# Performance work log

Measured on AMD Instinct MI355X. Metric: run time of the kernel, lower is better.

The kernel has to match this reference:

```python
import jax, jax.numpy as jnp
import numpy as np

NUM_NODES = 25
EMBED_DIM = 64
OUT_SIZE = 2
N_TOTAL = 204800   # 8192 graphs * 25 nodes
N_EDGES = 3276800  # avg degree 16


def setup_inputs() -> dict:
    key = jax.random.key(0)
    ks = jax.random.split(key, 8)
    x = jax.random.normal(ks[0], (N_TOTAL, EMBED_DIM), dtype=jnp.float32)
    # random edges; real graphs are graph-local but math is identical
    edge_index = jax.random.randint(ks[1], (2, N_EDGES), 0, N_TOTAL, dtype=jnp.int32)
    batch = jnp.repeat(jnp.arange(N_TOTAL // NUM_NODES, dtype=jnp.int32), NUM_NODES)
    hid = NUM_NODES * EMBED_DIM  # 1600
    W_conv = jax.random.normal(ks[2], (EMBED_DIM, EMBED_DIM), dtype=jnp.float32) / np.sqrt(EMBED_DIM)
    b_conv = jnp.zeros((EMBED_DIM,), dtype=jnp.float32)
    W1 = jax.random.normal(ks[3], (hid, hid), dtype=jnp.float32) / np.sqrt(hid)
    b1 = jnp.zeros((hid,), dtype=jnp.float32)
    W2 = jax.random.normal(ks[4], (hid, OUT_SIZE), dtype=jnp.float32) / np.sqrt(hid)
    b2 = jnp.zeros((OUT_SIZE,), dtype=jnp.float32)
    return {"x": x, "edge_index": edge_index, "batch": batch,
            "W_conv": W_conv, "b_conv": b_conv,
            "W1": W1, "b1": b1, "W2": W2, "b2": b2}


def reference(x, edge_index, batch, W_conv, b_conv, W1, b1, W2, b2):
    N = x.shape[0]
    # --- GCNConv: add self-loops, symmetric degree norm, transform, scatter-add ---
    loop = jnp.arange(N, dtype=edge_index.dtype)
    src = jnp.concatenate([edge_index[0], loop])
    dst = jnp.concatenate([edge_index[1], loop])
    deg = jax.ops.segment_sum(jnp.ones_like(dst, dtype=x.dtype), dst, num_segments=N)
    dinv = jax.lax.rsqrt(deg)  # deg >= 1 due to self-loops
    norm = dinv[src] * dinv[dst]                       # [E+N]
    h = x @ W_conv                                     # [N, D]
    msg = h[src] * norm[:, None]                       # gather + scale
    h = jax.ops.segment_sum(msg, dst, num_segments=N) + b_conv
    h = jax.nn.relu(h)
    # --- dense head ---
    nb = -(-batch.shape[0] // NUM_NODES)               # ceil
    h = h.reshape(nb, NUM_NODES * EMBED_DIM)           # [B, 1600]
    h = jax.nn.relu(h @ W1 + b1)
    logits = h @ W2 + b2
    return jax.nn.softmax(logits, axis=-1)
```

## Files before the change

kernel.cpp:

```cpp
#include <hip/hip_runtime.h>
#include <hip/hip_bf16.h>
#include <stdint.h>

#define NT   204800
#define NE   3276800
#define ED   64
#define NBG  8192
#define HID  1600
#define HPAD 1664
#define CAP  56
#define NBKT 400
#define BCAP 9216

typedef float  f32x4  __attribute__((ext_vector_type(4)));
typedef __bf16 bf16x8 __attribute__((ext_vector_type(8)));

__device__ __forceinline__ void async_ld16(const void* g, void* l) {
    __builtin_amdgcn_global_load_lds(
        (__attribute__((address_space(1))) const void*)g,
        (__attribute__((address_space(3))) void*)l, 16, 0, 0);
}

__device__ __forceinline__ unsigned short f2bf_raw(float f) {
    __hip_bfloat16 h = __float2bfloat16(f);
    return *(unsigned short*)&h;
}

__global__ void k_initg(int* __restrict__ gcur) {
    int t = threadIdx.x;
    if (t < NBKT) gcur[t] = t * BCAP;
}

__global__ __launch_bounds__(256) void k_part(const int* __restrict__ srcv,
                                              const int* __restrict__ dstv,
                                              int* __restrict__ gcur,
                                              unsigned* __restrict__ rec) {
    __shared__ int hist[NBKT];
    __shared__ int slot[NBKT];
    __shared__ int gofs[NBKT];
    const int t = threadIdx.x;
    const int base = blockIdx.x * (NE / 512);
    for (int i = t; i < NBKT; i += 256) { hist[i] = 0; slot[i] = 0; }
    __syncthreads();
    for (int j = 0; j < 25; ++j) {
        int d = dstv[base + j * 256 + t];
        atomicAdd(&hist[d >> 9], 1);
    }
    __syncthreads();
    for (int i = t; i < NBKT; i += 256) gofs[i] = atomicAdd(&gcur[i], hist[i]);
    __syncthreads();
    for (int j = 0; j < 25; ++j) {
        int i = base + j * 256 + t;
        int d = dstv[i];
        int s = srcv[i];
        int b = d >> 9;
        int ls = atomicAdd(&slot[b], 1);
        int idx = gofs[b] + ls;
        if (idx < (b + 1) * BCAP)
            rec[idx] = ((unsigned)s << 9) | (unsigned)(d & 511);
    }
}

__global__ __launch_bounds__(512) void k_fillb(const int* __restrict__ gcur,
                                               const unsigned* __restrict__ rec,
                                               int* __restrict__ cur,
                                               int* __restrict__ csr,
                                               float* __restrict__ dinv) {
    __shared__ int cnt[512];
    const int t = threadIdx.x;
    const int b = blockIdx.x;
    const int n0 = b * 512;
    cnt[t] = 0;
    __syncthreads();
    const int bstart = b * BCAP;
    int bcnt = gcur[b] - bstart;
    bcnt = (bcnt > BCAP) ? BCAP : bcnt;
    for (int idx = t; idx < bcnt; idx += 512) {
        unsigned r = rec[bstart + idx];
        unsigned rel = r & 511u;
        int ls = atomicAdd(&cnt[rel], 1);
        if (ls < CAP) csr[(size_t)(n0 + rel) * CAP + ls] = (int)(r >> 9);
    }
    __syncthreads();
    int cn = cnt[t];
    cur[n0 + t] = cn;
    dinv[n0 + t] = rsqrtf((float)cn + 1.f);
}

__global__ __launch_bounds__(256) void k_gemm_conv(const float* __restrict__ x,
                                                   const float* __restrict__ Wc,
                                                   const float* __restrict__ dinv,
                                                   __hip_bfloat16* __restrict__ hbs) {
    __shared__ unsigned short Xs[64 * 72];
    __shared__ unsigned short Wt[64 * 72];
    const int t = threadIdx.x;
    const int row0 = blockIdx.x * 64;
#pragma unroll
    for (int i = 0; i < 4; ++i) {
        int idx = i * 256 + t;
        int r = idx >> 4, c4 = (idx & 15) << 2;
        f32x4 wv = ((const f32x4*)Wc)[idx];
        Wt[(c4 + 0) * 72 + r] = f2bf_raw(wv.x);
        Wt[(c4 + 1) * 72 + r] = f2bf_raw(wv.y);
        Wt[(c4 + 2) * 72 + r] = f2bf_raw(wv.z);
        Wt[(c4 + 3) * 72 + r] = f2bf_raw(wv.w);
        f32x4 xv = ((const f32x4*)(x + (size_t)row0 * 64))[idx];
        ushort4 p;
        p.x = f2bf_raw(xv.x);
        p.y = f2bf_raw(xv.y);
        p.z = f2bf_raw(xv.z);
        p.w = f2bf_raw(xv.w);
        *(ushort4*)&Xs[r * 72 + c4] = p;
    }
    __syncthreads();
    const int w = t >> 6, lane = t & 63;
    const int fr = lane & 15, fq = lane >> 4;
    f32x4 acc[4] = {};
#pragma unroll
    for (int kb = 0; kb < 2; ++kb) {
        bf16x8 av = *(const bf16x8*)&Xs[(w * 16 + fr) * 72 + kb * 32 + fq * 8];
#pragma unroll
        for (int j = 0; j < 4; ++j) {
            bf16x8 bv = *(const bf16x8*)&Wt[(j * 16 + fr) * 72 + kb * 32 + fq * 8];
            acc[j] = __builtin_amdgcn_mfma_f32_16x16x32_bf16(av, bv, acc[j], 0, 0, 0);
        }
    }
#pragma unroll
    for (int r = 0; r < 4; ++r) {
        int row = row0 + w * 16 + fq * 4 + r;
        float di = dinv[row];
        unsigned short* dst = (unsigned short*)&hbs[(size_t)row * 64];
#pragma unroll
        for (int j = 0; j < 4; ++j)
            dst[j * 16 + fr] = f2bf_raw(acc[j][r] * di);
    }
}

__global__ __launch_bounds__(256) void k_gather(const int* __restrict__ cur,
                                                const int* __restrict__ csr,
                                                const float* __restrict__ dinv,
                                                const __hip_bfloat16* __restrict__ hbs,
                                                const float* __restrict__ bc,
                                                __hip_bfloat16* __restrict__ Hb) {
    const int lane = threadIdx.x & 63;
    const int d = blockIdx.x * 4 + (threadIdx.x >> 6);
    const float di = dinv[d];
    int cn = cur[d];
    cn = (cn > CAP) ? CAP : cn;
    int me = (lane < cn) ? __builtin_nontemporal_load(&csr[(size_t)d * CAP + lane]) : 0;
    float acc = __bfloat162float(hbs[(size_t)d * ED + lane]);
    int e = 0;
    for (; e + 8 <= cn; e += 8) {
        int s0 = __shfl(me, e,     64);
        int s1 = __shfl(me, e + 1, 64);
        int s2 = __shfl(me, e + 2, 64);
        int s3 = __shfl(me, e + 3, 64);
        int s4 = __shfl(me, e + 4, 64);
        int s5 = __shfl(me, e + 5, 64);
        int s6 = __shfl(me, e + 6, 64);
        int s7 = __shfl(me, e + 7, 64);
        float h0 = __bfloat162float(hbs[(size_t)s0 * ED + lane]);
        float h1 = __bfloat162float(hbs[(size_t)s1 * ED + lane]);
        float h2 = __bfloat162float(hbs[(size_t)s2 * ED + lane]);
        float h3 = __bfloat162float(hbs[(size_t)s3 * ED + lane]);
        float h4 = __bfloat162float(hbs[(size_t)s4 * ED + lane]);
        float h5 = __bfloat162float(hbs[(size_t)s5 * ED + lane]);
        float h6 = __bfloat162float(hbs[(size_t)s6 * ED + lane]);
        float h7 = __bfloat162float(hbs[(size_t)s7 * ED + lane]);
        acc += ((h0 + h1) + (h2 + h3)) + ((h4 + h5) + (h6 + h7));
    }
    for (; e < cn; ++e) {
        int s = __shfl(me, e, 64);
        acc += __bfloat162float(hbs[(size_t)s * ED + lane]);
    }
    Hb[(size_t)d * ED + lane] = __float2bfloat16(fmaxf(bc[lane] + di * acc, 0.f));
}

__global__ void k_convW1(const float* __restrict__ W1, __hip_bfloat16* __restrict__ Bt) {
    __shared__ float tile[64][65];
    const int t = threadIdx.x;
    const int k0 = blockIdx.x * 64;
    const int n0 = blockIdx.y * 64;
#pragma unroll
    for (int i = 0; i < 16; ++i) {
        int lin = i * 256 + t;
        int r = lin >> 6, c = lin & 63;
        int n = n0 + c;
        tile[r][c] = (n < HID) ? W1[(size_t)(k0 + r) * HID + n] : 0.f;
    }
    __syncthreads();
#pragma unroll
    for (int i = 0; i < 16; ++i) {
        int lin = i * 256 + t;
        int nn = lin >> 6, kk = lin & 63;
        Bt[(size_t)(n0 + nn) * HID + k0 + kk] = __float2bfloat16(tile[kk][nn]);
    }
}

__global__ __launch_bounds__(256) void k_gemm1(const __hip_bfloat16* __restrict__ A,
                                               const __hip_bfloat16* __restrict__ Bt,
                                               const float* __restrict__ b1,
                                               __hip_bfloat16* __restrict__ h2) {
    __shared__ unsigned short As[128 * 32];
    __shared__ unsigned short Bs[128 * 32];
    const int t = threadIdx.x;
    const int lane = t & 63;
    const int wave = t >> 6;
    const int bm0 = blockIdx.x * 128;
    const int bn0 = blockIdx.y * 128;
    const int wm = (wave >> 1) * 64;
    const int wn = (wave & 1) * 64;
    const int fr = lane & 15;
    const int fq = lane >> 4;
    const int sr = t >> 2;
    const int sc = (t & 3) * 8;
    const __hip_bfloat16* ga0 = A + (size_t)(bm0 + sr) * HID + sc;
    const __hip_bfloat16* ga1 = A + (size_t)(bm0 + 64 + sr) * HID + sc;
    const __hip_bfloat16* gb0 = Bt + (size_t)(bn0 + sr) * HID + sc;
    const __hip_bfloat16* gb1 = Bt + (size_t)(bn0 + 64 + sr) * HID + sc;
    unsigned short* lA0 = &As[t * 8];
    unsigned short* lA1 = &As[(256 + t) * 8];
    unsigned short* lB0 = &Bs[t * 8];
    unsigned short* lB1 = &Bs[(256 + t) * 8];
    const unsigned short* fa0 = &As[(wm + fr) * 32 + fq * 8];
    const unsigned short* fb0 = &Bs[(wn + fr) * 32 + fq * 8];
    f32x4 acc[4][4] = {};
    for (int k0 = 0; k0 < HID; k0 += 32) {
        async_ld16(ga0, lA0); async_ld16(ga1, lA1);
        async_ld16(gb0, lB0); async_ld16(gb1, lB1);
        ga0 += 32; ga1 += 32; gb0 += 32; gb1 += 32;
        __syncthreads();
        bf16x8 av[4], bv[4];
#pragma unroll
        for (int i = 0; i < 4; ++i) av[i] = *(const bf16x8*)(fa0 + i * 16 * 32);
#pragma unroll
        for (int j = 0; j < 4; ++j) bv[j] = *(const bf16x8*)(fb0 + j * 16 * 32);
#pragma unroll
        for (int i = 0; i < 4; ++i)
#pragma unroll
            for (int j = 0; j < 4; ++j)
                acc[i][j] = __builtin_amdgcn_mfma_f32_16x16x32_bf16(av[i], bv[j], acc[i][j], 0, 0, 0);
        __syncthreads();
    }
#pragma unroll
    for (int j = 0; j < 4; ++j) {
        int n = bn0 + wn + j * 16 + fr;
        if (n < HID) {
            float bias = b1[n];
#pragma unroll
            for (int i = 0; i < 4; ++i) {
#pragma unroll
                for (int r = 0; r < 4; ++r) {
                    int m = bm0 + wm + i * 16 + fq * 4 + r;
                    float v = acc[i][j][r] + bias;
                    h2[(size_t)m * HID + n] = __float2bfloat16(fmaxf(v, 0.f));
                }
            }
        }
    }
}

__global__ void k_head(const __hip_bfloat16* __restrict__ h2, const float* __restrict__ W2,
                       const float* __restrict__ b2, float* __restrict__ out) {
    int g = blockIdx.x * 4 + (threadIdx.x >> 6);
    int lane = threadIdx.x & 63;
    const __hip_bfloat16* row = h2 + (size_t)g * HID;
    float a0 = 0.f, a1 = 0.f;
#pragma unroll
    for (int i = 0; i < 25; ++i) {
        int k = i * 64 + lane;
        float hv = __bfloat162float(row[k]);
        float2 w = ((const float2*)W2)[k];
        a0 += hv * w.x;
        a1 += hv * w.y;
    }
#pragma unroll
    for (int off = 32; off > 0; off >>= 1) {
        a0 += __shfl_down(a0, off, 64);
        a1 += __shfl_down(a1, off, 64);
    }
    if (lane == 0) {
        float l0 = a0 + b2[0], l1 = a1 + b2[1];
        float mx = fmaxf(l0, l1);
        float e0 = expf(l0 - mx), e1 = expf(l1 - mx);
        float s = e0 + e1;
        out[2 * g]     = e0 / s;
        out[2 * g + 1] = e1 / s;
    }
}

extern "C" void kernel_launch(void* const* d_in, const int* in_sizes, int n_in,
                              void* d_out, int out_size, void* d_ws, size_t ws_size,
                              hipStream_t stream) {
    const float* x  = (const float*)d_in[0];
    const int*   ei = (const int*)d_in[1];
    const float* Wc = (const float*)d_in[3];
    const float* bc = (const float*)d_in[4];
    const float* W1 = (const float*)d_in[5];
    const float* b1 = (const float*)d_in[6];
    const float* W2 = (const float*)d_in[7];
    const float* b2 = (const float*)d_in[8];
    float* out = (float*)d_out;

    const int* srcv = ei;
    const int* dstv = ei + NE;

    char* ws = (char*)d_ws;
    int*   cur  = (int*)ws;
    float* dinv = (float*)(ws + 819200);
    int*   gcur = (int*)(ws + 1638400);
    int*   csr  = (int*)(ws + 1642496);
    unsigned* rec = (unsigned*)(ws + 47517696);
    __hip_bfloat16* hbs = (__hip_bfloat16*)(ws + 47517696);
    __hip_bfloat16* h2  = (__hip_bfloat16*)(ws + 47517696);
    __hip_bfloat16* Hb  = (__hip_bfloat16*)(ws + 73732096);
    __hip_bfloat16* Bt  = (__hip_bfloat16*)(ws + 99946496);

    k_initg    <<<1, 512, 0, stream>>>(gcur);
    k_part     <<<512, 256, 0, stream>>>(srcv, dstv, gcur, rec);
    k_fillb    <<<NBKT, 512, 0, stream>>>(gcur, rec, cur, csr, dinv);
    k_gemm_conv<<<NT / 64, 256, 0, stream>>>(x, Wc, dinv, hbs);
    k_gather   <<<NT / 4, 256, 0, stream>>>(cur, csr, dinv, hbs, bc, Hb);
    k_convW1   <<<dim3(HID / 64, HPAD / 64), 256, 0, stream>>>(W1, Bt);
    k_gemm1    <<<dim3(NBG / 128, HPAD / 128), 256, 0, stream>>>(Hb, Bt, b1, h2);
    k_head     <<<NBG / 4, 256, 0, stream>>>(h2, W2, b2, out);
}
```

Baseline: 412.7 us.

## Fuse W2 projection into GEMM1 epilogue and sort fill records by source tile

The GEMM1 epilogue now applies bias and ReLU and dots each row with W2 in registers, reducing across lanes and atomically adding into a small logits buffer. This avoids writing and re-reading the bf16 hidden activations. A lightweight softmax kernel replaces the head. Separately, the CSR fill kernel first sorts each bucket's records by source range in shared memory so the CSR writes and later gathers gain locality, at the cost of an extra pass and float atomics whose summation order is nondeterministic.

```diff
diff --git a/kernel.cpp b/kernel.cpp
--- a/kernel.cpp
+++ b/kernel.cpp
@@ -11,6 +11,7 @@
 #define CAP  56
 #define NBKT 400
 #define BCAP 9216
+#define NTL  50
 
 typedef float  f32x4  __attribute__((ext_vector_type(4)));
 typedef __bf16 bf16x8 __attribute__((ext_vector_type(8)));
@@ -26,9 +27,10 @@
     return *(unsigned short*)&h;
 }
 
-__global__ void k_initg(int* __restrict__ gcur) {
-    int t = threadIdx.x;
-    if (t < NBKT) gcur[t] = t * BCAP;
+__global__ void k_init(int* __restrict__ gcur, float* __restrict__ logits) {
+    int i = blockIdx.x * 256 + threadIdx.x;
+    if (i < NBKT) gcur[i] = i * BCAP;
+    logits[i] = 0.f;
 }
 
 __global__ __launch_bounds__(256) void k_part(const int* __restrict__ srcv,
@@ -66,17 +68,34 @@
                                                int* __restrict__ cur,
                                                int* __restrict__ csr,
                                                float* __restrict__ dinv) {
+    __shared__ unsigned rs[BCAP];
+    __shared__ int hist[NTL];
+    __shared__ int ofs[NTL];
     __shared__ int cnt[512];
     const int t = threadIdx.x;
     const int b = blockIdx.x;
     const int n0 = b * 512;
+    if (t < NTL) hist[t] = 0;
     cnt[t] = 0;
     __syncthreads();
-    const int bstart = b * BCAP;
-    int bcnt = gcur[b] - bstart;
+    const unsigned* gr = rec + (size_t)b * BCAP;
+    int bcnt = gcur[b] - b * BCAP;
     bcnt = (bcnt > BCAP) ? BCAP : bcnt;
-    for (int idx = t; idx < bcnt; idx += 512) {
-        unsigned r = rec[bstart + idx];
+    for (int i = t; i < bcnt; i += 512) atomicAdd(&hist[gr[i] >> 21], 1);
+    __syncthreads();
+    if (t == 0) {
+        int a = 0;
+        for (int i = 0; i < NTL; ++i) { ofs[i] = a; a += hist[i]; }
+    }
+    __syncthreads();
+    for (int i = t; i < bcnt; i += 512) {
+        unsigned r = gr[i];
+        int p = atomicAdd(&ofs[r >> 21], 1);
+        rs[p] = r;
+    }
+    __syncthreads();
+    for (int i = t; i < bcnt; i += 512) {
+        unsigned r = rs[i];
         unsigned rel = r & 511u;
         int ls = atomicAdd(&cnt[rel], 1);
         if (ls < CAP) csr[(size_t)(n0 + rel) * CAP + ls] = (int)(r >> 9);
@@ -200,7 +219,8 @@
 __global__ __launch_bounds__(256) void k_gemm1(const __hip_bfloat16* __restrict__ A,
                                                const __hip_bfloat16* __restrict__ Bt,
                                                const float* __restrict__ b1,
-                                               __hip_bfloat16* __restrict__ h2) {
+                                               const float* __restrict__ W2,
+                                               float* __restrict__ logits) {
     __shared__ unsigned short As[128 * 32];
     __shared__ unsigned short Bs[128 * 32];
     const int t = threadIdx.x;
@@ -242,51 +262,50 @@
                 acc[i][j] = __builtin_amdgcn_mfma_f32_16x16x32_bf16(av[i], bv[j], acc[i][j], 0, 0, 0);
         __syncthreads();
     }
+    float biasj[4], w2x[4], w2y[4];
 #pragma unroll
     for (int j = 0; j < 4; ++j) {
         int n = bn0 + wn + j * 16 + fr;
         if (n < HID) {
-            float bias = b1[n];
-#pragma unroll
-            for (int i = 0; i < 4; ++i) {
-#pragma unroll
-                for (int r = 0; r < 4; ++r) {
-                    int m = bm0 + wm + i * 16 + fq * 4 + r;
-                    float v = acc[i][j][r] + bias;
-                    h2[(size_t)m * HID + n] = __float2bfloat16(fmaxf(v, 0.f));
-                }
+            biasj[j] = b1[n];
+            float2 w = ((const float2*)W2)[n];
+            w2x[j] = w.x; w2y[j] = w.y;
+        } else { biasj[j] = 0.f; w2x[j] = 0.f; w2y[j] = 0.f; }
+    }
+#pragma unroll
+    for (int i = 0; i < 4; ++i) {
+#pragma unroll
+        for (int r = 0; r < 4; ++r) {
+            float a0 = 0.f, a1 = 0.f;
+#pragma unroll
+            for (int j = 0; j < 4; ++j) {
+                float v = fmaxf(acc[i][j][r] + biasj[j], 0.f);
+                a0 += v * w2x[j];
+                a1 += v * w2y[j];
+            }
+            a0 += __shfl_xor(a0, 1, 64); a1 += __shfl_xor(a1, 1, 64);
+            a0 += __shfl_xor(a0, 2, 64); a1 += __shfl_xor(a1, 2, 64);
+            a0 += __shfl_xor(a0, 4, 64); a1 += __shfl_xor(a1, 4, 64);
+            a0 += __shfl_xor(a0, 8, 64); a1 += __shfl_xor(a1, 8, 64);
+            if (fr == 0) {
+                int m = bm0 + wm + i * 16 + fq * 4 + r;
+                unsafeAtomicAdd(&logits[2 * m],     a0);
+                unsafeAtomicAdd(&logits[2 * m + 1], a1);
             }
         }
     }
 }
 
-__global__ void k_head(const __hip_bfloat16* __restrict__ h2, const float* __restrict__ W2,
-                       const float* __restrict__ b2, float* __restrict__ out) {
-    int g = blockIdx.x * 4 + (threadIdx.x >> 6);
-    int lane = threadIdx.x & 63;
-    const __hip_bfloat16* row = h2 + (size_t)g * HID;
-    float a0 = 0.f, a1 = 0.f;
-#pragma unroll
-    for (int i = 0; i < 25; ++i) {
-        int k = i * 64 + lane;
-        float hv = __bfloat162float(row[k]);
-        float2 w = ((const float2*)W2)[k];
-        a0 += hv * w.x;
-        a1 += hv * w.y;
-    }
-#pragma unroll
-    for (int off = 32; off > 0; off >>= 1) {
-        a0 += __shfl_down(a0, off, 64);
-        a1 += __shfl_down(a1, off, 64);
-    }
-    if (lane == 0) {
-        float l0 = a0 + b2[0], l1 = a1 + b2[1];
-        float mx = fmaxf(l0, l1);
-        float e0 = expf(l0 - mx), e1 = expf(l1 - mx);
-        float s = e0 + e1;
-        out[2 * g]     = e0 / s;
-        out[2 * g + 1] = e1 / s;
-    }
+__global__ void k_soft(const float* __restrict__ logits, const float* __restrict__ b2,
+                       float* __restrict__ out) {
+    int g = blockIdx.x * 256 + threadIdx.x;
+    float l0 = logits[2 * g]     + b2[0];
+    float l1 = logits[2 * g + 1] + b2[1];
+    float mx = fmaxf(l0, l1);
+    float e0 = expf(l0 - mx), e1 = expf(l1 - mx);
+    float s = e0 + e1;
+    out[2 * g]     = e0 / s;
+    out[2 * g + 1] = e1 / s;
 }
 
 extern "C" void kernel_launch(void* const* d_in, const int* in_sizes, int n_in,
@@ -312,16 +331,16 @@
     int*   csr  = (int*)(ws + 1642496);
     unsigned* rec = (unsigned*)(ws + 47517696);
     __hip_bfloat16* hbs = (__hip_bfloat16*)(ws + 47517696);
-    __hip_bfloat16* h2  = (__hip_bfloat16*)(ws + 47517696);
     __hip_bfloat16* Hb  = (__hip_bfloat16*)(ws + 73732096);
     __hip_bfloat16* Bt  = (__hip_bfloat16*)(ws + 99946496);
-
-    k_initg    <<<1, 512, 0, stream>>>(gcur);
+    float* logits = (float*)(ws + 105271296);
+
+    k_init     <<<64, 256, 0, stream>>>(gcur, logits);
     k_part     <<<512, 256, 0, stream>>>(srcv, dstv, gcur, rec);
     k_fillb    <<<NBKT, 512, 0, stream>>>(gcur, rec, cur, csr, dinv);
     k_gemm_conv<<<NT / 64, 256, 0, stream>>>(x, Wc, dinv, hbs);
     k_gather   <<<NT / 4, 256, 0, stream>>>(cur, csr, dinv, hbs, bc, Hb);
     k_convW1   <<<dim3(HID / 64, HPAD / 64), 256, 0, stream>>>(W1, Bt);
-    k_gemm1    <<<dim3(NBG / 128, HPAD / 128), 256, 0, stream>>>(Hb, Bt, b1, h2);
-    k_head     <<<NBG / 4, 256, 0, stream>>>(h2, W2, b2, out);
-}
+    k_gemm1    <<<dim3(NBG / 128, HPAD / 128), 256, 0, stream>>>(Hb, Bt, b1, W2, logits);
+    k_soft     <<<NBG / 256, 256, 0, stream>>>(logits, b2, out);
+}
```

Result: no change. 414.0 us (+0.3%).
